# Performance work log

Measured on AMD Instinct MI355X. Metric: run time of the kernel, lower is better.

## Reference

```python
import jax, jax.numpy as jnp
import numpy as np

VOXEL_SIZE = (0.2, 0.2)
GX, GY = 512, 512
MAX_PTS = 32  # max_points_per_pillar
IN_CH = 4


def setup_inputs() -> dict:
    key = jax.random.key(0)
    k1, k2 = jax.random.split(key)
    N, B = 400000, 2
    extent = GX * VOXEL_SIZE[0]  # 102.4 -> points land inside the grid
    all_points = jax.random.uniform(k1, (N, IN_CH), dtype=jnp.float32) * extent
    batch_indices = jnp.sort(jax.random.randint(k2, (N,), 0, B))
    return {"all_points": all_points, "batch_indices": batch_indices, "num_point_clouds": B}


def reference(all_points, batch_indices, num_point_clouds):
    B, P, C = num_point_clouds, MAX_PTS, all_points.shape[1]
    G = B * GX * GY  # total pillar slots
    vs = jnp.array(VOXEL_SIZE, dtype=all_points.dtype)
    # torch .long() truncates toward zero; points are non-negative here
    xy = (all_points[:, :2] / vs).astype(jnp.int32)
    xy = jnp.clip(xy, 0, jnp.array([GX - 1, GY - 1], dtype=jnp.int32))
    bidx = batch_indices.astype(jnp.int32)
    flat = bidx * (GX * GY) + xy[:, 0] * GY + xy[:, 1]  # [N]
    # counts per pillar (torch.unique + scatter_add equivalent)
    counts_full = jax.ops.segment_sum(jnp.ones_like(flat), flat, num_segments=G)
    occupied = counts_full > 0
    # torch.unique inverse index = rank of the pillar among occupied pillars
    inverse_full = jnp.cumsum(occupied.astype(jnp.int32)) - 1  # [G]
    inverse = inverse_full[flat]                               # [N]
    # drop ALL points of over-full pillars (count > P), as the original mask does
    mask = counts_full[flat] <= P
    pos = jnp.arange(flat.shape[0], dtype=jnp.int32)
    last_pos = jax.ops.segment_max(jnp.where(mask, pos, -1), inverse, num_segments=G)
    occ = last_pos >= 0
    winner = jnp.where(occ[:, None], all_points[jnp.clip(last_pos, 0)], 0.0)  # [G, C]
    # [M,C] assigned into [M,P,C] broadcasts over the P slot dim in torch
    voxel_features = jnp.broadcast_to(winner[:, None, :], (G, P, C)).reshape(B, GX, GY, P, C)
    # original allocates voxel_counts but never writes it
    voxel_counts = jnp.zeros((B, GX, GY), dtype=jnp.int32)
    return voxel_features, voxel_counts
```

## Files before the change

kernel.cpp:

```cpp
#include <hip/hip_runtime.h>

#define GXv 512
#define GYv 512
#define PMAX 32

typedef float vfloat4 __attribute__((ext_vector_type(4)));
typedef int   vint4   __attribute__((ext_vector_type(4)));


__global__ void zero_kernel(vint4* __restrict__ counts4, int n4) {
    int i = blockIdx.x * blockDim.x + threadIdx.x;
    if (i < n4) counts4[i] = (vint4)0;
}

__global__ void points_kernel(const float4* __restrict__ pts, const int* __restrict__ bidx,
                              int* __restrict__ counts, int* __restrict__ lastp, int N) {
    int i = blockIdx.x * blockDim.x + threadIdx.x;
    if (i >= N) return;
    float4 p = pts[i];
    int x = (int)(p.x / 0.2f);
    int y = (int)(p.y / 0.2f);
    x = min(max(x, 0), GXv - 1);
    y = min(max(y, 0), GYv - 1);
    int flat = bidx[i] * (GXv * GYv) + x * GYv + y;
    atomicAdd(&counts[flat], 1);
    atomicMax(&lastp[flat], i + 1);
}

__global__ void blocksum_kernel(const int* __restrict__ counts, int* __restrict__ bs) {
    int t = threadIdx.x, b = blockIdx.x;
    int2 c = ((const int2*)counts)[b * 256 + t];
    __shared__ int sm[256];
    sm[t] = (c.x > 0) + (c.y > 0);
    __syncthreads();
    for (int off = 128; off > 0; off >>= 1) {
        if (t < off) sm[t] += sm[t + off];
        __syncthreads();
    }
    if (t == 0) bs[b] = sm[0];
}

__global__ __launch_bounds__(256) void scatter_kernel(
        const int* __restrict__ counts, const int* __restrict__ lastp,
        const int* __restrict__ bs, const vfloat4* __restrict__ pts,
        vfloat4* __restrict__ out, int G, int SB) {
    __shared__ int sm[256];
    __shared__ int smb[256];
    __shared__ vfloat4 pil[512];
    int t = threadIdx.x, b = blockIdx.x;
    int2 c2 = ((const int2*)counts)[b * 256 + t];
    int2 lp2 = ((const int2*)lastp)[b * 256 + t];
    int occ0 = (c2.x > 0), occ1 = (c2.y > 0);

    sm[t] = occ0 + occ1;
    __syncthreads();
    for (int off = 1; off < 256; off <<= 1) {
        int a = (t >= off) ? sm[t - off] : 0;
        __syncthreads();
        sm[t] += a;
        __syncthreads();
    }
    int excl = (t == 0) ? 0 : sm[t - 1];
    int aggL = sm[255];
    __syncthreads();

    int s_all = 0, s_below = 0;
    for (int i = t; i < SB; i += 256) {
        int v = bs[i];
        s_all += v;
        if (i < b) s_below += v;
    }
    sm[t] = s_all;
    smb[t] = s_below;
    __syncthreads();
    for (int off = 128; off > 0; off >>= 1) {
        if (t < off) { sm[t] += sm[t + off]; smb[t] += smb[t + off]; }
        __syncthreads();
    }
    int M = sm[0];
    size_t base = (size_t)smb[0] * 32;
    __syncthreads();

    if (occ0) pil[excl]        = (c2.x <= PMAX) ? pts[lp2.x - 1] : (vfloat4)0;
    if (occ1) pil[excl + occ0] = (c2.y <= PMAX) ? pts[lp2.y - 1] : (vfloat4)0;
    __syncthreads();

    int n = aggL * 32;
    for (int j = t; j < n; j += 256) {
        vfloat4 v = pil[j >> 5];
        __builtin_nontemporal_store(v, &out[base + (size_t)j]);
    }

    size_t idx = (size_t)M * 32 + (size_t)b * 256 + t;
    size_t end = (size_t)G * 32 + (size_t)(G / 4);
    size_t stride = (size_t)SB * 256;
    vfloat4 z = (vfloat4)0;
    for (; idx < end; idx += stride)
        __builtin_nontemporal_store(z, &out[idx]);
}

extern "C" void kernel_launch(void* const* d_in, const int* in_sizes, int n_in,
                              void* d_out, int out_size, void* d_ws, size_t ws_size,
                              hipStream_t stream) {
    const float4* pts = (const float4*)d_in[0];
    const int* bidx = (const int*)d_in[1];
    int N = in_sizes[0] / 4;
    int G = out_size / 129;
    int SB = G / 512;

    int* counts = (int*)d_ws;
    int* lastp = counts + G;
    int* bs = lastp + G;
    vfloat4* out = (vfloat4*)d_out;

    int n4 = G / 4;
    zero_kernel<<<(n4 + 255) / 256, 256, 0, stream>>>((vint4*)counts, n4);
    points_kernel<<<(N + 255) / 256, 256, 0, stream>>>(pts, bidx, counts, lastp, N);
    blocksum_kernel<<<SB, 256, 0, stream>>>(counts, bs);
    scatter_kernel<<<SB, 256, 0, stream>>>(counts, lastp, bs, (const vfloat4*)pts, out, G, SB);
}
```

Measured before the change: 318.3 us.

## Zero the whole output inside the points kernel and drop tail zeroing from scatter

```diff
diff --git a/kernel.cpp b/kernel.cpp
--- a/kernel.cpp
+++ b/kernel.cpp
@@ -13,18 +13,27 @@
     if (i < n4) counts4[i] = (vint4)0;
 }
 
-__global__ void points_kernel(const float4* __restrict__ pts, const int* __restrict__ bidx,
-                              int* __restrict__ counts, int* __restrict__ lastp, int N) {
+__global__ __launch_bounds__(256) void points_zero_kernel(
+        const float4* __restrict__ pts, const int* __restrict__ bidx,
+        int* __restrict__ counts, int* __restrict__ lastp,
+        vfloat4* __restrict__ out, int N, int total4) {
     int i = blockIdx.x * blockDim.x + threadIdx.x;
-    if (i >= N) return;
-    float4 p = pts[i];
-    int x = (int)(p.x / 0.2f);
-    int y = (int)(p.y / 0.2f);
-    x = min(max(x, 0), GXv - 1);
-    y = min(max(y, 0), GYv - 1);
-    int flat = bidx[i] * (GXv * GYv) + x * GYv + y;
-    atomicAdd(&counts[flat], 1);
-    atomicMax(&lastp[flat], i + 1);
+    int GT = gridDim.x * blockDim.x;
+
+    if (i < N) {
+        float4 p = pts[i];
+        int x = (int)(p.x / 0.2f);
+        int y = (int)(p.y / 0.2f);
+        x = min(max(x, 0), GXv - 1);
+        y = min(max(y, 0), GYv - 1);
+        int flat = bidx[i] * (GXv * GYv) + x * GYv + y;
+        atomicAdd(&counts[flat], 1);
+        atomicMax(&lastp[flat], i + 1);
+    }
+
+    vfloat4 z = (vfloat4)0;
+    for (int j = i; j < total4; j += GT)
+        __builtin_nontemporal_store(z, &out[j]);
 }
 
 __global__ void blocksum_kernel(const int* __restrict__ counts, int* __restrict__ bs) {
@@ -43,9 +52,8 @@
 __global__ __launch_bounds__(256) void scatter_kernel(
         const int* __restrict__ counts, const int* __restrict__ lastp,
         const int* __restrict__ bs, const vfloat4* __restrict__ pts,
-        vfloat4* __restrict__ out, int G, int SB) {
+        vfloat4* __restrict__ out, int SB) {
     __shared__ int sm[256];
-    __shared__ int smb[256];
     __shared__ vfloat4 pil[512];
     int t = threadIdx.x, b = blockIdx.x;
     int2 c2 = ((const int2*)counts)[b * 256 + t];
@@ -64,21 +72,15 @@
     int aggL = sm[255];
     __syncthreads();
 
-    int s_all = 0, s_below = 0;
-    for (int i = t; i < SB; i += 256) {
-        int v = bs[i];
-        s_all += v;
-        if (i < b) s_below += v;
-    }
-    sm[t] = s_all;
-    smb[t] = s_below;
+    int s_below = 0;
+    for (int i = t; i < b; i += 256) s_below += bs[i];
+    sm[t] = s_below;
     __syncthreads();
     for (int off = 128; off > 0; off >>= 1) {
-        if (t < off) { sm[t] += sm[t + off]; smb[t] += smb[t + off]; }
+        if (t < off) sm[t] += sm[t + off];
         __syncthreads();
     }
-    int M = sm[0];
-    size_t base = (size_t)smb[0] * 32;
+    size_t base = (size_t)sm[0] * 32;
     __syncthreads();
 
     if (occ0) pil[excl]        = (c2.x <= PMAX) ? pts[lp2.x - 1] : (vfloat4)0;
@@ -90,13 +92,6 @@
         vfloat4 v = pil[j >> 5];
         __builtin_nontemporal_store(v, &out[base + (size_t)j]);
     }
-
-    size_t idx = (size_t)M * 32 + (size_t)b * 256 + t;
-    size_t end = (size_t)G * 32 + (size_t)(G / 4);
-    size_t stride = (size_t)SB * 256;
-    vfloat4 z = (vfloat4)0;
-    for (; idx < end; idx += stride)
-        __builtin_nontemporal_store(z, &out[idx]);
 }
 
 extern "C" void kernel_launch(void* const* d_in, const int* in_sizes, int n_in,
@@ -115,7 +110,11 @@
 
     int n4 = G / 4;
     zero_kernel<<<(n4 + 255) / 256, 256, 0, stream>>>((vint4*)counts, n4);
-    points_kernel<<<(N + 255) / 256, 256, 0, stream>>>(pts, bidx, counts, lastp, N);
+
+    int total4 = out_size / 4;
+    int nb2 = (N + 255) / 256;
+    points_zero_kernel<<<nb2, 256, 0, stream>>>(pts, bidx, counts, lastp, out, N, total4);
+
     blocksum_kernel<<<SB, 256, 0, stream>>>(counts, bs);
-    scatter_kernel<<<SB, 256, 0, stream>>>(counts, lastp, bs, (const vfloat4*)pts, out, G, SB);
+    scatter_kernel<<<SB, 256, 0, stream>>>(counts, lastp, bs, (const vfloat4*)pts, out, SB);
 }
```

Measured after the change: 321.2 us. About the same (+0.9%).
